# Kernel optimization log

Measured on AMD Instinct MI355X. Metric: run time of the kernel, lower is better.

## Reference

```python
import jax, jax.numpy as jnp
import numpy as np

DIM = 192; HEADS = 6; WS = 7; RES = 56; SHIFT = 3
HEAD_DIM = DIM // HEADS
SCALE = HEAD_DIM ** -0.5
N = WS * WS
EPS = 1e-5

def _rel_pos_index():
    coords = np.stack(np.meshgrid(np.arange(WS), np.arange(WS), indexing='ij')).reshape(2, -1)
    rel = coords[:, :, None] - coords[:, None, :]  # [2,N,N]
    rel = rel.transpose(1, 2, 0)
    rel[:, :, 0] += WS - 1
    rel[:, :, 1] += WS - 1
    rel[:, :, 0] *= 2 * WS - 1
    return rel.sum(-1)  # [N,N]

def _attn_mask():
    img = np.zeros((RES, RES), dtype=np.float32)
    slices = (slice(0, -WS), slice(-WS, -SHIFT), slice(-SHIFT, None))
    cnt = 0
    for h in slices:
        for w in slices:
            img[h, w] = cnt; cnt += 1
    mw = img.reshape(RES // WS, WS, RES // WS, WS).transpose(0, 2, 1, 3).reshape(-1, N)  # [nW,N]
    diff = mw[:, None, :] - mw[:, :, None]
    return np.where(diff != 0, -100.0, 0.0).astype(np.float32)  # [nW,N,N]

REL_IDX = jnp.asarray(_rel_pos_index())
ATTN_MASK = jnp.asarray(_attn_mask())

def _ln(x, g, b):
    mu = x.mean(-1, keepdims=True)
    var = ((x - mu) ** 2).mean(-1, keepdims=True)
    return (x - mu) * jax.lax.rsqrt(var + EPS) * g + b

def setup_inputs() -> dict:
    key = jax.random.key(0)
    ks = jax.random.split(key, 8)
    d = {
        'x': jax.random.normal(ks[0], (32, RES * RES, DIM), jnp.float32),
        'norm1_g': jnp.ones((DIM,), jnp.float32), 'norm1_b': jnp.zeros((DIM,), jnp.float32),
        'qkv_w': jax.random.normal(ks[1], (DIM, 3 * DIM), jnp.float32) * 0.02,
        'qkv_b': jnp.zeros((3 * DIM,), jnp.float32),
        'proj_w': jax.random.normal(ks[2], (DIM, DIM), jnp.float32) * 0.02,
        'proj_b': jnp.zeros((DIM,), jnp.float32),
        'bias_table': jax.random.normal(ks[3], ((2 * WS - 1) ** 2, HEADS), jnp.float32) * 0.02,
        'norm2_g': jnp.ones((DIM,), jnp.float32), 'norm2_b': jnp.zeros((DIM,), jnp.float32),
        'fc1_w': jax.random.normal(ks[4], (DIM, 4 * DIM), jnp.float32) * 0.02,
        'fc1_b': jnp.zeros((4 * DIM,), jnp.float32),
        'fc2_w': jax.random.normal(ks[5], (4 * DIM, DIM), jnp.float32) * 0.02,
        'fc2_b': jnp.zeros((DIM,), jnp.float32),
    }
    return d

def reference(x, norm1_g, norm1_b, qkv_w, qkv_b, proj_w, proj_b, bias_table,
              norm2_g, norm2_b, fc1_w, fc1_b, fc2_w, fc2_b):
    B, L, C = x.shape
    H = W = RES
    shortcut = x
    h = _ln(x, norm1_g, norm1_b).reshape(B, H, W, C)
    # cyclic shift
    h = jnp.roll(h, (-SHIFT, -SHIFT), axis=(1, 2))
    # window partition -> [B*nW, N, C]
    nH = H // WS
    h = h.reshape(B, nH, WS, nH, WS, C).transpose(0, 1, 3, 2, 4, 5).reshape(-1, N, C)
    BW = h.shape[0]
    # windowed MHSA
    qkv = (h @ qkv_w + qkv_b).reshape(BW, N, 3, HEADS, HEAD_DIM)
    q, k, v = qkv[:, :, 0], qkv[:, :, 1], qkv[:, :, 2]  # [BW,N,h,hd]
    attn = jnp.einsum('bnhd,bmhd->bhnm', q, k) * SCALE  # [BW,h,N,N]
    bias = bias_table[REL_IDX.reshape(-1)].reshape(N, N, HEADS).transpose(2, 0, 1)
    attn = attn + bias[None]
    nW = ATTN_MASK.shape[0]
    attn = attn.reshape(BW // nW, nW, HEADS, N, N) + ATTN_MASK[None, :, None]
    attn = jax.nn.softmax(attn.reshape(BW, HEADS, N, N), axis=-1)
    h = jnp.einsum('bhnm,bmhd->bnhd', attn, v).reshape(BW, N, C)
    h = h @ proj_w + proj_b
    # window reverse
    h = h.reshape(B, nH, nH, WS, WS, C).transpose(0, 1, 3, 2, 4, 5).reshape(B, H, W, C)
    h = jnp.roll(h, (SHIFT, SHIFT), axis=(1, 2)).reshape(B, L, C)
    x = shortcut + h
    # MLP
    m = _ln(x, norm2_g, norm2_b)
    m = jax.nn.gelu(m @ fc1_w + fc1_b, approximate=False) @ fc2_w + fc2_b
    return x + m
```

## Files before the change

kernel.cpp:

```cpp
#include <hip/hip_runtime.h>
#include <hip/hip_bf16.h>
#include <math.h>

typedef __attribute__((ext_vector_type(8))) short bh8;
typedef __attribute__((ext_vector_type(4))) float fx4;

__device__ __forceinline__ fx4 mfma_bf16(bh8 a, bh8 b, fx4 c) {
    return __builtin_amdgcn_mfma_f32_16x16x32_bf16(a, b, c, 0, 0, 0);
}

__device__ __forceinline__ void gload16(const __hip_bfloat16* g, __hip_bfloat16* l) {
    __builtin_amdgcn_global_load_lds(
        (const __attribute__((address_space(1))) void*)g,
        (__attribute__((address_space(3))) void*)l,
        16, 0, 0);
}

__global__ __launch_bounds__(256)
void convw_k(const float* __restrict__ W, __hip_bfloat16* __restrict__ Wt, int K, int Nn)
{
    int idx = blockIdx.x * 256 + threadIdx.x;
    if (idx < K * Nn) {
        int k = idx / Nn, n = idx - k * Nn;
        Wt[(size_t)n * K + k] = __float2bfloat16(W[idx]);
    }
}

__global__ __launch_bounds__(256)
void ln1_gather_k(const float* __restrict__ x, const float* __restrict__ g,
                  const float* __restrict__ bia, __hip_bfloat16* __restrict__ xw)
{
    const int wave = threadIdx.x >> 6, lane = threadIdx.x & 63;
    const int t = blockIdx.x * 4 + wave;
    const int w = t / 49, n = t - w * 49;
    const int b = w >> 6, wrem = w & 63, wi = wrem >> 3, wj = wrem & 7;
    const int i = n / 7, j = n - i * 7;
    int sr = wi * 7 + i + 3; if (sr >= 56) sr -= 56;
    int sc = wj * 7 + j + 3; if (sc >= 56) sc -= 56;
    const float* xp = x + ((size_t)b * 3136 + sr * 56 + sc) * 192;
    float v0 = xp[lane], v1 = xp[lane + 64], v2 = xp[lane + 128];
    float s = v0 + v1 + v2;
    float q = v0 * v0 + v1 * v1 + v2 * v2;
    for (int off = 32; off > 0; off >>= 1) {
        s += __shfl_down(s, off, 64);
        q += __shfl_down(q, off, 64);
    }
    s = __shfl(s, 0, 64); q = __shfl(q, 0, 64);
    float mean = s * (1.0f / 192.0f);
    float var  = q * (1.0f / 192.0f) - mean * mean;
    float rstd = rsqrtf(var + 1e-5f);
    __hip_bfloat16* op = xw + (size_t)t * 192;
    op[lane]       = __float2bfloat16((v0 - mean) * rstd * g[lane]       + bia[lane]);
    op[lane + 64]  = __float2bfloat16((v1 - mean) * rstd * g[lane + 64]  + bia[lane + 64]);
    op[lane + 128] = __float2bfloat16((v2 - mean) * rstd * g[lane + 128] + bia[lane + 128]);
}

template<int MODE, int K, int NOUT>
__global__ __launch_bounds__(256)
void gemm2_k(const __hip_bfloat16* __restrict__ A,
             const __hip_bfloat16* __restrict__ Bt,
             const float* __restrict__ bias,
             const float* __restrict__ resid,
             void* __restrict__ outv)
{
    __shared__ __align__(16) __hip_bfloat16 As[128 * 32];
    __shared__ __align__(16) __hip_bfloat16 Bs[64 * 32];
    const int tid  = threadIdx.x;
    const int lane = tid & 63, wave = tid >> 6;
    const int quad = lane >> 4, l15 = lane & 15;
    const int m0 = blockIdx.x * 128, n0 = blockIdx.y * 64;

    const int arow = lane >> 2, acol = (lane & 3) * 8;
    const __hip_bfloat16* Ag0 = A  + (size_t)(m0 + wave * 32 + arow)      * K + acol;
    const __hip_bfloat16* Ag1 = A  + (size_t)(m0 + wave * 32 + 16 + arow) * K + acol;
    const __hip_bfloat16* Bg  = Bt + (size_t)(n0 + wave * 16 + arow)      * K + acol;
    __hip_bfloat16* Al0 = &As[(wave * 32)      * 32];
    __hip_bfloat16* Al1 = &As[(wave * 32 + 16) * 32];
    __hip_bfloat16* Bl  = &Bs[(wave * 16)      * 32];

    fx4 acc[2][4];
#pragma unroll
    for (int mi = 0; mi < 2; mi++)
#pragma unroll
        for (int ni = 0; ni < 4; ni++) acc[mi][ni] = {0.f, 0.f, 0.f, 0.f};

    for (int k0 = 0; k0 < K; k0 += 32) {
        gload16(Ag0 + k0, Al0);
        gload16(Ag1 + k0, Al1);
        gload16(Bg  + k0, Bl);
        __syncthreads();
        bh8 a0 = *(const bh8*)&As[(wave * 32 + l15)      * 32 + quad * 8];
        bh8 a1 = *(const bh8*)&As[(wave * 32 + 16 + l15) * 32 + quad * 8];
        bh8 b0 = *(const bh8*)&Bs[(0 * 16 + l15) * 32 + quad * 8];
        bh8 b1 = *(const bh8*)&Bs[(1 * 16 + l15) * 32 + quad * 8];
        bh8 b2 = *(const bh8*)&Bs[(2 * 16 + l15) * 32 + quad * 8];
        bh8 b3 = *(const bh8*)&Bs[(3 * 16 + l15) * 32 + quad * 8];
        acc[0][0] = mfma_bf16(a0, b0, acc[0][0]);
        acc[0][1] = mfma_bf16(a0, b1, acc[0][1]);
        acc[0][2] = mfma_bf16(a0, b2, acc[0][2]);
        acc[0][3] = mfma_bf16(a0, b3, acc[0][3]);
        acc[1][0] = mfma_bf16(a1, b0, acc[1][0]);
        acc[1][1] = mfma_bf16(a1, b1, acc[1][1]);
        acc[1][2] = mfma_bf16(a1, b2, acc[1][2]);
        acc[1][3] = mfma_bf16(a1, b3, acc[1][3]);
        __syncthreads();
    }

#pragma unroll
    for (int mi = 0; mi < 2; mi++)
#pragma unroll
    for (int ni = 0; ni < 4; ni++) {
        const int n = n0 + ni * 16 + l15;
        const float bn = bias[n];
#pragma unroll
        for (int r = 0; r < 4; r++) {
            const int m = m0 + wave * 32 + mi * 16 + quad * 4 + r;
            float v = acc[mi][ni][r] + bn;
            if (MODE == 0) {
                if (n < 192) v *= 0.17677669529663687f;
                ((__hip_bfloat16*)outv)[(size_t)m * NOUT + n] = __float2bfloat16(v);
            } else if (MODE == 2) {
                v = 0.5f * v * (1.0f + erff(v * 0.70710678118654752f));
                ((__hip_bfloat16*)outv)[(size_t)m * NOUT + n] = __float2bfloat16(v);
            } else {
                ((float*)outv)[(size_t)m * NOUT + n] = v + resid[(size_t)m * NOUT + n];
            }
        }
    }
}

__global__ __launch_bounds__(256)
void projln_k(const __hip_bfloat16* __restrict__ A,
              const __hip_bfloat16* __restrict__ Bt,
              const float* __restrict__ pb,
              const float* __restrict__ xresid,
              const float* __restrict__ g2,
              const float* __restrict__ b2,
              float* __restrict__ x1out,
              __hip_bfloat16* __restrict__ y2out)
{
    __shared__ __align__(16) __hip_bfloat16 As[64 * 32];
    __shared__ __align__(16) __hip_bfloat16 Bs[192 * 32];
    const int tid  = threadIdx.x;
    const int lane = tid & 63, wave = tid >> 6;
    const int quad = lane >> 4, l15 = lane & 15;
    const int m0 = blockIdx.x * 64;

    const int arow = lane >> 2, acol = (lane & 3) * 8;
    const __hip_bfloat16* Ag = A + (size_t)(m0 + wave * 16 + arow) * 192 + acol;
    __hip_bfloat16* Al = &As[(wave * 16) * 32];
    const __hip_bfloat16* Bg0 = Bt + (size_t)((wave + 0) * 16 + arow) * 192 + acol;
    const __hip_bfloat16* Bg1 = Bt + (size_t)((wave + 4) * 16 + arow) * 192 + acol;
    const __hip_bfloat16* Bg2 = Bt + (size_t)((wave + 8) * 16 + arow) * 192 + acol;
    __hip_bfloat16* Bl0 = &Bs[((wave + 0) * 16) * 32];
    __hip_bfloat16* Bl1 = &Bs[((wave + 4) * 16) * 32];
    __hip_bfloat16* Bl2 = &Bs[((wave + 8) * 16) * 32];

    fx4 acc[12];
#pragma unroll
    for (int ct = 0; ct < 12; ct++) acc[ct] = {0.f, 0.f, 0.f, 0.f};

    for (int k0 = 0; k0 < 192; k0 += 32) {
        gload16(Ag  + k0, Al);
        gload16(Bg0 + k0, Bl0);
        gload16(Bg1 + k0, Bl1);
        gload16(Bg2 + k0, Bl2);
        __syncthreads();
        bh8 a = *(const bh8*)&As[(wave * 16 + l15) * 32 + quad * 8];
#pragma unroll
        for (int ct = 0; ct < 12; ct++) {
            bh8 b = *(const bh8*)&Bs[(ct * 16 + l15) * 32 + quad * 8];
            acc[ct] = mfma_bf16(a, b, acc[ct]);
        }
        __syncthreads();
    }

#pragma unroll
    for (int r = 0; r < 4; r++) {
        const int row = m0 + wave * 16 + quad * 4 + r;
        float vv[12];
        float s = 0.f, q = 0.f;
#pragma unroll
        for (int ct = 0; ct < 12; ct++) {
            const int col = ct * 16 + l15;
            float v = acc[ct][r] + pb[col] + xresid[(size_t)row * 192 + col];
            vv[ct] = v;
            x1out[(size_t)row * 192 + col] = v;
            s += v;
            q += v * v;
        }
        s += __shfl_xor(s, 1, 64);  q += __shfl_xor(q, 1, 64);
        s += __shfl_xor(s, 2, 64);  q += __shfl_xor(q, 2, 64);
        s += __shfl_xor(s, 4, 64);  q += __shfl_xor(q, 4, 64);
        s += __shfl_xor(s, 8, 64);  q += __shfl_xor(q, 8, 64);
        float mean = s * (1.0f / 192.0f);
        float var  = q * (1.0f / 192.0f) - mean * mean;
        float rstd = rsqrtf(var + 1e-5f);
#pragma unroll
        for (int ct = 0; ct < 12; ct++) {
            const int col = ct * 16 + l15;
            float y = (vv[ct] - mean) * rstd * g2[col] + b2[col];
            y2out[(size_t)row * 192 + col] = __float2bfloat16(y);
        }
    }
}

__global__ __launch_bounds__(256)
void attn_k(const __hip_bfloat16* __restrict__ qkv,
            const float* __restrict__ bias_table,
            __hip_bfloat16* __restrict__ aout)
{
    __shared__ __align__(16) __hip_bfloat16 Qb[64 * 32];
    __shared__ __align__(16) __hip_bfloat16 Kb[64 * 32];
    __shared__ __align__(16) __hip_bfloat16 Vt[32 * 64];
    __shared__ __align__(16) __hip_bfloat16 Ps[64 * 72];
    __shared__ float bias_h[169];

    const int tid  = threadIdx.x;
    const int lane = tid & 63, wave = tid >> 6;
    const int quad = lane >> 4, l15 = lane & 15;
    const int w = blockIdx.x / 6, hd = blockIdx.x % 6;
    const int b = w >> 6, wrem = w & 63, wi = wrem >> 3, wj = wrem & 7;
    const size_t base = (size_t)w * 49 * 576 + hd * 32;

    if (tid < 169) bias_h[tid] = bias_table[tid * 6 + hd];

    bh8 z = {0, 0, 0, 0, 0, 0, 0, 0};
    {
        int row = tid >> 2, ch = (tid & 3) * 8;
        if (row < 49) {
            *(bh8*)&Qb[row * 32 + ch] = *(const bh8*)(qkv + base + (size_t)row * 576 + ch);
            *(bh8*)&Kb[row * 32 + ch] = *(const bh8*)(qkv + base + (size_t)row * 576 + 192 + ch);
        } else {
            *(bh8*)&Qb[row * 32 + ch] = z;
            *(bh8*)&Kb[row * 32 + ch] = z;
        }
        *(bh8*)&Vt[tid * 8] = z;
    }
    __syncthreads();
    for (int idx = tid; idx < 49 * 32; idx += 256) {
        int n = idx >> 5, d = idx & 31;
        Vt[d * 64 + n] = qkv[base + (size_t)n * 576 + 384 + d];
    }
    __syncthreads();

    fx4 zf = {0.f, 0.f, 0.f, 0.f};
    bh8 aq = *(const bh8*)&Qb[(wave * 16 + l15) * 32 + quad * 8];
    fx4 sarr[4];
#pragma unroll
    for (int ni = 0; ni < 4; ni++) {
        bh8 bk = *(const bh8*)&Kb[(ni * 16 + l15) * 32 + quad * 8];
        sarr[ni] = mfma_bf16(aq, bk, zf);
    }

    int iarr[4], ria[4], cia[4], mbi[4];
#pragma unroll
    for (int r = 0; r < 4; r++) {
        int i = wave * 16 + quad * 4 + r;
        int ri = i / 7, ci = i - ri * 7;
        iarr[r] = i; ria[r] = ri; cia[r] = ci;
        int ar = wi * 7 + ri, ac = wj * 7 + ci;
        int br = (ar < 49) ? 0 : ((ar < 53) ? 1 : 2);
        int bc = (ac < 49) ? 0 : ((ac < 53) ? 1 : 2);
        mbi[r] = br * 3 + bc;
    }
    float vals[4][4];
#pragma unroll
    for (int ni = 0; ni < 4; ni++) {
        int jcol = ni * 16 + l15;
        int rj = jcol / 7, cj = jcol - rj * 7;
        int ar = wi * 7 + rj, ac = wj * 7 + cj;
        int br = (ar < 49) ? 0 : ((ar < 53) ? 1 : 2);
        int bc = (ac < 49) ? 0 : ((ac < 53) ? 1 : 2);
        int mbj = br * 3 + bc;
#pragma unroll
        for (int r = 0; r < 4; r++) {
            float v;
            if (jcol >= 49)            v = -1e30f;
            else if (iarr[r] >= 49)    v = 0.0f;
            else {
                int bidx = (ria[r] - rj + 6) * 13 + (cia[r] - cj + 6);
                v = sarr[ni][r] + bias_h[bidx] + ((mbi[r] != mbj) ? -100.0f : 0.0f);
            }
            vals[ni][r] = v;
        }
    }
#pragma unroll
    for (int r = 0; r < 4; r++) {
        float mx = fmaxf(fmaxf(vals[0][r], vals[1][r]), fmaxf(vals[2][r], vals[3][r]));
        mx = fmaxf(mx, __shfl_xor(mx, 1, 64));
        mx = fmaxf(mx, __shfl_xor(mx, 2, 64));
        mx = fmaxf(mx, __shfl_xor(mx, 4, 64));
        mx = fmaxf(mx, __shfl_xor(mx, 8, 64));
        float e0 = __expf(vals[0][r] - mx);
        float e1 = __expf(vals[1][r] - mx);
        float e2 = __expf(vals[2][r] - mx);
        float e3 = __expf(vals[3][r] - mx);
        float sm = e0 + e1 + e2 + e3;
        sm += __shfl_xor(sm, 1, 64);
        sm += __shfl_xor(sm, 2, 64);
        sm += __shfl_xor(sm, 4, 64);
        sm += __shfl_xor(sm, 8, 64);
        float inv = 1.0f / sm;
        int prow = (wave * 16 + quad * 4 + r) * 72;
        Ps[prow + 0 * 16 + l15] = __float2bfloat16(e0 * inv);
        Ps[prow + 1 * 16 + l15] = __float2bfloat16(e1 * inv);
        Ps[prow + 2 * 16 + l15] = __float2bfloat16(e2 * inv);
        Ps[prow + 3 * 16 + l15] = __float2bfloat16(e3 * inv);
    }
    __syncthreads();

    fx4 o0 = zf, o1 = zf;
#pragma unroll
    for (int k0 = 0; k0 < 64; k0 += 32) {
        bh8 ap  = *(const bh8*)&Ps[(wave * 16 + l15) * 72 + k0 + quad * 8];
        bh8 bv0 = *(const bh8*)&Vt[(l15)      * 64 + k0 + quad * 8];
        bh8 bv1 = *(const bh8*)&Vt[(16 + l15) * 64 + k0 + quad * 8];
        o0 = mfma_bf16(ap, bv0, o0);
        o1 = mfma_bf16(ap, bv1, o1);
    }

#pragma unroll
    for (int r = 0; r < 4; r++) {
        int m = wave * 16 + quad * 4 + r;
        if (m < 49) {
            int i = m / 7, j2 = m - i * 7;
            int orow = wi * 7 + i + 3;  if (orow >= 56) orow -= 56;
            int ocol = wj * 7 + j2 + 3; if (ocol >= 56) ocol -= 56;
            size_t t = (size_t)b * 3136 + orow * 56 + ocol;
            aout[t * 192 + hd * 32 + l15]      = __float2bfloat16(o0[r]);
            aout[t * 192 + hd * 32 + 16 + l15] = __float2bfloat16(o1[r]);
        }
    }
}

extern "C" void kernel_launch(void* const* d_in, const int* in_sizes, int n_in,
                              void* d_out, int out_size, void* d_ws, size_t ws_size,
                              hipStream_t stream)
{
    const float* x      = (const float*)d_in[0];
    const float* n1g    = (const float*)d_in[1];
    const float* n1b    = (const float*)d_in[2];
    const float* qkv_w  = (const float*)d_in[3];
    const float* qkv_b  = (const float*)d_in[4];
    const float* proj_w = (const float*)d_in[5];
    const float* proj_b = (const float*)d_in[6];
    const float* btab   = (const float*)d_in[7];
    const float* n2g    = (const float*)d_in[8];
    const float* n2b    = (const float*)d_in[9];
    const float* fc1_w  = (const float*)d_in[10];
    const float* fc1_b  = (const float*)d_in[11];
    const float* fc2_w  = (const float*)d_in[12];
    const float* fc2_b  = (const float*)d_in[13];

    char* ws = (char*)d_ws;
    __hip_bfloat16* buf1    = (__hip_bfloat16*)(ws + 0);
    __hip_bfloat16* buf2    = (__hip_bfloat16*)(ws + 38535168);
    __hip_bfloat16* wt_qkv  = (__hip_bfloat16*)(ws + 192675840);
    __hip_bfloat16* wt_proj = (__hip_bfloat16*)(ws + 192897024);
    __hip_bfloat16* wt_fc1  = (__hip_bfloat16*)(ws + 192970752);
    __hip_bfloat16* wt_fc2  = (__hip_bfloat16*)(ws + 193265664);
    float*          x1      = (float*)d_out;

    convw_k<<<dim3(432), 256, 0, stream>>>(qkv_w, wt_qkv, 192, 576);
    convw_k<<<dim3(144), 256, 0, stream>>>(proj_w, wt_proj, 192, 192);
    convw_k<<<dim3(576), 256, 0, stream>>>(fc1_w, wt_fc1, 192, 768);
    convw_k<<<dim3(576), 256, 0, stream>>>(fc2_w, wt_fc2, 768, 192);

    ln1_gather_k<<<dim3(25088), 256, 0, stream>>>(x, n1g, n1b, buf1);

    gemm2_k<0, 192, 576><<<dim3(784, 9), 256, 0, stream>>>(buf1, wt_qkv, qkv_b, nullptr, buf2);

    attn_k<<<dim3(12288), 256, 0, stream>>>(buf2, btab, buf1);

    projln_k<<<dim3(1568), 256, 0, stream>>>(buf1, wt_proj, proj_b, x, n2g, n2b, x1, buf1);

    gemm2_k<2, 192, 768><<<dim3(784, 12), 256, 0, stream>>>(buf1, wt_fc1, fc1_b, nullptr, buf2);

    gemm2_k<3, 768, 192><<<dim3(784, 3), 256, 0, stream>>>(buf2, wt_fc2, fc2_b, x1, x1);
}
```

Baseline: 552.9 us.

## Fuse fc1+GELU+fc2 MLP into one kernel keeping hidden activations on-chip

Replaces the two MLP GEMM launches with a single kernel. Each block owns 64 rows and streams the 768-wide hidden dimension in 64-column chunks: fc1 plus GELU goes into shared memory, then is immediately multiplied by the matching fc2 slice and accumulated in registers. This avoids writing and re-reading the bf16 hidden tensor in global memory. In exchange it reloads all weights per block with no double-buffering, serialises loads and compute with barriers, and each wave does only 16 rows, so occupancy and MFMA utilisation may suffer.

```diff
diff --git a/kernel.cpp b/kernel.cpp
--- a/kernel.cpp
+++ b/kernel.cpp
@@ -125,6 +125,110 @@
             } else {
                 ((float*)outv)[(size_t)m * NOUT + n] = v + resid[(size_t)m * NOUT + n];
             }
+        }
+    }
+}
+
+__global__ __launch_bounds__(256)
+void mlp_k(const __hip_bfloat16* __restrict__ A,
+           const __hip_bfloat16* __restrict__ W1t,
+           const __hip_bfloat16* __restrict__ W2t,
+           const float* __restrict__ b1,
+           const float* __restrict__ b2,
+           float* __restrict__ out)
+{
+    __shared__ __align__(16) __hip_bfloat16 Xs[6][64][32];
+    __shared__ __align__(16) __hip_bfloat16 W1s[6][64][32];
+    __shared__ __align__(16) __hip_bfloat16 W2s[2][192][32];
+    __shared__ __align__(16) __hip_bfloat16 Hs[2][64][32];
+
+    const int tid  = threadIdx.x;
+    const int lane = tid & 63, wave = tid >> 6;
+    const int quad = lane >> 4, l15 = lane & 15;
+    const int m0 = blockIdx.x * 64;
+    const int arow = lane >> 2, acol = (lane & 3) * 8;
+
+    const __hip_bfloat16* xg  = A   + (size_t)(m0 + wave * 16 + arow) * 192 + acol;
+    const __hip_bfloat16* w1g = W1t + (size_t)(wave * 16 + arow) * 192 + acol;
+    const __hip_bfloat16* w2g = W2t + (size_t)(wave * 48 + arow) * 768 + acol;
+
+#pragma unroll
+    for (int kc = 0; kc < 6; kc++) {
+        gload16(xg  + kc * 32, &Xs[kc][wave * 16][0]);
+        gload16(w1g + kc * 32, &W1s[kc][wave * 16][0]);
+    }
+#pragma unroll
+    for (int i = 0; i < 3; i++)
+#pragma unroll
+        for (int hc = 0; hc < 2; hc++)
+            gload16(w2g + (size_t)i * 16 * 768 + hc * 32, &W2s[hc][wave * 48 + i * 16][0]);
+    __syncthreads();
+
+    fx4 acc2[12];
+#pragma unroll
+    for (int nt = 0; nt < 12; nt++) acc2[nt] = {0.f, 0.f, 0.f, 0.f};
+
+    for (int c = 0; c < 12; c++) {
+        float b1v[4];
+#pragma unroll
+        for (int ni = 0; ni < 4; ni++) b1v[ni] = b1[c * 64 + ni * 16 + l15];
+
+        fx4 acc1[4];
+#pragma unroll
+        for (int ni = 0; ni < 4; ni++) acc1[ni] = {0.f, 0.f, 0.f, 0.f};
+#pragma unroll
+        for (int kc = 0; kc < 6; kc++) {
+            bh8 a = *(const bh8*)&Xs[kc][wave * 16 + l15][quad * 8];
+#pragma unroll
+            for (int ni = 0; ni < 4; ni++) {
+                bh8 b = *(const bh8*)&W1s[kc][ni * 16 + l15][quad * 8];
+                acc1[ni] = mfma_bf16(a, b, acc1[ni]);
+            }
+        }
+#pragma unroll
+        for (int ni = 0; ni < 4; ni++) {
+#pragma unroll
+            for (int r = 0; r < 4; r++) {
+                float v = acc1[ni][r] + b1v[ni];
+                v = 0.5f * v * (1.0f + erff(v * 0.70710678118654752f));
+                Hs[ni >> 1][wave * 16 + quad * 4 + r][(ni & 1) * 16 + l15] = __float2bfloat16(v);
+            }
+        }
+        asm volatile("s_waitcnt lgkmcnt(0)" ::: "memory");
+        __builtin_amdgcn_sched_barrier(0);
+
+#pragma unroll
+        for (int hc = 0; hc < 2; hc++) {
+            bh8 ap = *(const bh8*)&Hs[hc][wave * 16 + l15][quad * 8];
+#pragma unroll
+            for (int nt = 0; nt < 12; nt++) {
+                bh8 b = *(const bh8*)&W2s[hc][nt * 16 + l15][quad * 8];
+                acc2[nt] = mfma_bf16(ap, b, acc2[nt]);
+            }
+        }
+        __syncthreads();
+        if (c < 11) {
+#pragma unroll
+            for (int kc = 0; kc < 6; kc++)
+                gload16(w1g + (size_t)(c + 1) * 64 * 192 + kc * 32, &W1s[kc][wave * 16][0]);
+#pragma unroll
+            for (int i = 0; i < 3; i++)
+#pragma unroll
+                for (int hc = 0; hc < 2; hc++)
+                    gload16(w2g + (size_t)i * 16 * 768 + (c + 1) * 64 + hc * 32,
+                            &W2s[hc][wave * 48 + i * 16][0]);
+            __syncthreads();
+        }
+    }
+
+#pragma unroll
+    for (int nt = 0; nt < 12; nt++) {
+        const int n = nt * 16 + l15;
+        const float bn = b2[n];
+#pragma unroll
+        for (int r = 0; r < 4; r++) {
+            const int m = m0 + wave * 16 + quad * 4 + r;
+            out[(size_t)m * 192 + n] += acc2[nt][r] + bn;
         }
     }
 }
@@ -375,7 +479,5 @@
 
     projln_k<<<dim3(1568), 256, 0, stream>>>(buf1, wt_proj, proj_b, x, n2g, n2b, x1, buf1);
 
-    gemm2_k<2, 192, 768><<<dim3(784, 12), 256, 0, stream>>>(buf1, wt_fc1, fc1_b, nullptr, buf2);
-
-    gemm2_k<3, 768, 192><<<dim3(784, 3), 256, 0, stream>>>(buf2, wt_fc2, fc2_b, x1, x1);
-}
+    mlp_k<<<dim3(1568), 256, 0, stream>>>(buf1, wt_fc1, wt_fc2, fc1_b, fc2_b, x1);
+}
```

Result: faster. 511.1 us (-7.6%).
